# Optimization experiments

Measured on AMD Instinct MI355X. Metric: run time of the kernel, lower is better.

Reference implementation:

```python
import jax, jax.numpy as jnp
import numpy as np

D_MODEL = 128
N_HEADS = 8
D_HEAD = D_MODEL // N_HEADS
D_EDGE = 32
D_GATE = max(D_EDGE * 2, 64)
N_NODES = 50000
N_EDGES = 800000


def setup_inputs() -> dict:
    key = jax.random.key(0)
    ks = jax.random.split(key, 11)
    s = 1.0 / np.sqrt(D_MODEL)
    se = 1.0 / np.sqrt(D_EDGE)
    sg = 1.0 / np.sqrt(D_GATE)
    return {
        "x": jax.random.normal(ks[0], (N_NODES, D_MODEL), jnp.float32),
        "edge_index": jax.random.randint(ks[1], (2, N_EDGES), 0, N_NODES, jnp.int64) if jax.config.jax_enable_x64 else jax.random.randint(ks[1], (2, N_EDGES), 0, N_NODES, jnp.int32),
        "edge_attr": jax.random.normal(ks[2], (N_EDGES, D_EDGE), jnp.float32),
        "W_q": jax.random.normal(ks[3], (D_MODEL, D_MODEL), jnp.float32) * s,
        "W_k": jax.random.normal(ks[4], (D_MODEL, D_MODEL), jnp.float32) * s,
        "W_v": jax.random.normal(ks[5], (D_MODEL, D_MODEL), jnp.float32) * s,
        "W_o": jax.random.normal(ks[6], (D_MODEL, D_MODEL), jnp.float32) * s,
        "W_ek": jax.random.normal(ks[7], (D_EDGE, D_MODEL), jnp.float32) * se,
        "W_ev": jax.random.normal(ks[8], (D_EDGE, D_MODEL), jnp.float32) * se,
        "W_g1": jax.random.normal(ks[9], (D_EDGE, D_GATE), jnp.float32) * se,
        "W_g2": jax.random.normal(ks[10], (D_GATE, N_HEADS), jnp.float32) * sg,
    }


def reference(x, edge_index, edge_attr, W_q, W_k, W_v, W_o, W_ek, W_ev, W_g1, W_g2):
    N = x.shape[0]
    E = edge_attr.shape[0]
    H, D = N_HEADS, D_HEAD
    src, dst = edge_index[0], edge_index[1]

    q = (x @ W_q).reshape(N, H, D)
    k = (x @ W_k).reshape(N, H, D)
    v = (x @ W_v).reshape(N, H, D)

    # per-edge gather + edge-feature enrichment of K, V
    q_e = q[dst]                                        # [E,H,D]
    k_e = k[src] + (edge_attr @ W_ek).reshape(E, H, D)  # [E,H,D]
    v_e = v[src] + (edge_attr @ W_ev).reshape(E, H, D)  # [E,H,D]

    scale = jnp.asarray(np.sqrt(D), x.dtype)
    gate = jax.nn.silu(edge_attr @ W_g1) @ W_g2         # [E,H]
    scores = jnp.sum(q_e * k_e, axis=-1) / scale + gate  # [E,H]

    # 3-pass scatter segment softmax over destination nodes
    m = jax.ops.segment_max(scores, dst, num_segments=N)   # [N,H]
    exp_s = jnp.exp(scores - m[dst])                        # [E,H]
    denom = jax.ops.segment_sum(exp_s, dst, num_segments=N)  # [N,H]
    att = exp_s / (denom[dst] + 1e-9)                       # [E,H]

    out = jax.ops.segment_sum(att[..., None] * v_e, dst, num_segments=N)  # [N,H,D]
    return out.reshape(N, H * D) @ W_o
```

## Files before the change

### kernel.cpp

```cpp
#include <hip/hip_runtime.h>

#define NN 50000
#define NP 50048
#define NE 800000
#define DM 128
#define NH 8
#define DE 32
#define DG 64
#define MAXDEG 64
#define LOG2E 1.44269504088896f
#define SHIFT 16.0f

typedef __attribute__((ext_vector_type(8))) short bf16x8;
typedef __attribute__((ext_vector_type(4))) float f32x4;
typedef __attribute__((ext_vector_type(2))) float f32x2;

__device__ __forceinline__ unsigned short f2bf(float f) {
    unsigned u = __float_as_uint(f);
    unsigned r = u + 0x7FFFu + ((u >> 16) & 1u);
    return (unsigned short)(r >> 16);
}

__global__ void k_prep(const float* __restrict__ Wq, const float* __restrict__ Wk,
                       const float* __restrict__ Wv, unsigned short* __restrict__ wt,
                       const float* __restrict__ Wo, unsigned short* __restrict__ wto,
                       const float* __restrict__ Wek, float* __restrict__ WekT,
                       const float* __restrict__ Wg1, unsigned short* __restrict__ wg1t,
                       const float* __restrict__ Wg2, unsigned short* __restrict__ wg2t,
                       int* __restrict__ cnt) {
    int idx = blockIdx.x * 256 + threadIdx.x;
    if (idx < 3 * DM * DM) {
        int m = idx >> 14, rem = idx & 16383, c = rem >> 7, kk = rem & 127;
        const float* W = m == 0 ? Wq : (m == 1 ? Wk : Wv);
        wt[idx] = f2bf(W[kk * DM + c]);
    }
    if (idx < DM * DM) {
        int c = idx >> 7, kk = idx & 127;
        wto[idx] = f2bf(Wo[kk * DM + c]);
    }
    if (idx < DE * DM) {
        int d = idx >> 5, i = idx & 31;
        WekT[idx] = Wek[i * DM + d];
    }
    if (idx < DG * DE) {
        int c = idx >> 5, kk = idx & 31;
        wg1t[idx] = f2bf(Wg1[kk * DG + c]);
    }
    if (idx < 16 * DG) {
        int c = idx >> 6, kk = idx & 63;
        wg2t[idx] = (c < NH) ? f2bf(Wg2[kk * NH + c]) : (unsigned short)0;
    }
    if (idx < NN) cnt[idx] = 0;
}

__global__ __launch_bounds__(256) void k_qkv(
    const float* __restrict__ x, const unsigned short* __restrict__ wt,
    float* __restrict__ q, unsigned* __restrict__ kvp) {
    int lane = threadIdx.x & 63;
    int w = threadIdx.x >> 6;
    int rt = blockIdx.x * 64 + w * 16;
    int cl = lane & 15;
    int kc = (lane >> 4) * 8;
    bool valid = (rt + cl) < NN;
    bf16x8 a[4];
    #pragma unroll
    for (int ks = 0; ks < 4; ++ks) {
        float4 f0 = make_float4(0.f, 0.f, 0.f, 0.f), f1 = f0;
        if (valid) {
            const float* xp = x + (size_t)(rt + cl) * DM + ks * 32 + kc;
            f0 = *(const float4*)xp;
            f1 = *(const float4*)(xp + 4);
        }
        bf16x8 av;
        av[0] = (short)f2bf(f0.x); av[1] = (short)f2bf(f0.y);
        av[2] = (short)f2bf(f0.z); av[3] = (short)f2bf(f0.w);
        av[4] = (short)f2bf(f1.x); av[5] = (short)f2bf(f1.y);
        av[6] = (short)f2bf(f1.z); av[7] = (short)f2bf(f1.w);
        a[ks] = av;
    }
    int r0w = rt + (lane >> 4) * 4;
    const float QSC = 0.25f * LOG2E;
    #pragma unroll
    for (int m = 0; m < 3; ++m) {
        const unsigned short* wtm = wt + m * DM * DM;
        f32x4 acc[8];
        #pragma unroll
        for (int j = 0; j < 8; ++j) acc[j] = (f32x4){0.f, 0.f, 0.f, 0.f};
        #pragma unroll
        for (int j = 0; j < 8; ++j) {
            #pragma unroll
            for (int ks = 0; ks < 4; ++ks) {
                bf16x8 b = *(const bf16x8*)(wtm + (size_t)(j * 16 + cl) * DM + ks * 32 + kc);
                acc[j] = __builtin_amdgcn_mfma_f32_16x16x32_bf16(a[ks], b, acc[j], 0, 0, 0);
            }
        }
        if (m == 0) {
            #pragma unroll
            for (int j = 0; j < 8; ++j)
                #pragma unroll
                for (int r = 0; r < 4; ++r)
                    q[(size_t)(r0w + r) * DM + j * 16 + cl] = acc[j][r] * QSC;
        } else {
            #pragma unroll
            for (int j = 0; j < 4; ++j)
                #pragma unroll
                for (int r = 0; r < 4; ++r) {
                    unsigned pk = (unsigned)f2bf(acc[j][r]) | ((unsigned)f2bf(acc[j + 4][r]) << 16);
                    kvp[(size_t)(r0w + r) * DM + 2 * (j * 16 + cl) + (m - 1)] = pk;
                }
        }
    }
}

__global__ __launch_bounds__(256) void k_qwek(
    const float* __restrict__ q, const float* __restrict__ WekT,
    unsigned* __restrict__ qwekh) {
    int t = threadIdx.x & 127;
    int sub = threadIdx.x >> 7;
    int h = t >> 4, i2 = t & 15;
    float wk0[16], wk1[16];
    #pragma unroll
    for (int d = 0; d < 16; ++d) {
        wk0[d] = WekT[(h * 16 + d) * 32 + 2 * i2];
        wk1[d] = WekT[(h * 16 + d) * 32 + 2 * i2 + 1];
    }
    for (int n = blockIdx.x * 2 + sub; n < NN; n += gridDim.x * 2) {
        const float4* qr = (const float4*)(q + (size_t)n * DM + h * 16);
        float a0 = 0.f, a1 = 0.f;
        #pragma unroll
        for (int c = 0; c < 4; ++c) {
            float4 qq = qr[c];
            a0 += qq.x * wk0[4*c] + qq.y * wk0[4*c+1] + qq.z * wk0[4*c+2] + qq.w * wk0[4*c+3];
            a1 += qq.x * wk1[4*c] + qq.y * wk1[4*c+1] + qq.z * wk1[4*c+2] + qq.w * wk1[4*c+3];
        }
        qwekh[(size_t)n * 128 + h * 16 + i2] = (unsigned)f2bf(a0) | ((unsigned)f2bf(a1) << 16);
    }
}

__global__ __launch_bounds__(256) void k_edge(
    const float* __restrict__ ea,
    const unsigned short* __restrict__ wg1t, const unsigned short* __restrict__ wg2t,
    const int* __restrict__ ei, int* __restrict__ cnt,
    int2* __restrict__ eb, float2* __restrict__ g2, unsigned* __restrict__ eah) {
    __shared__ unsigned short hls[4][16 * 64];
    int lane = threadIdx.x & 63;
    int wv = threadIdx.x >> 6;
    int e0 = (blockIdx.x * 4 + wv) * 16;
    int cl = lane & 15;
    int g = lane >> 4;
    int kc = g * 8;

    const float* ear = ea + (size_t)(e0 + cl) * DE + kc;
    float4 f0 = *(const float4*)ear;
    float4 f1 = *(const float4*)(ear + 4);
    bf16x8 a;
    a[0] = (short)f2bf(f0.x); a[1] = (short)f2bf(f0.y);
    a[2] = (short)f2bf(f0.z); a[3] = (short)f2bf(f0.w);
    a[4] = (short)f2bf(f1.x); a[5] = (short)f2bf(f1.y);
    a[6] = (short)f2bf(f1.z); a[7] = (short)f2bf(f1.w);
    *(bf16x8*)(eah + (size_t)(e0 + cl) * 16 + kc / 2) = a;

    f32x4 hC[4];
    #pragma unroll
    for (int j = 0; j < 4; ++j) {
        bf16x8 b = *(const bf16x8*)(wg1t + (size_t)(j * 16 + cl) * DE + kc);
        hC[j] = __builtin_amdgcn_mfma_f32_16x16x32_bf16(a, b, (f32x4){0.f, 0.f, 0.f, 0.f}, 0, 0, 0);
    }

    unsigned short* hw = hls[wv];
    #pragma unroll
    for (int j = 0; j < 4; ++j) {
        #pragma unroll
        for (int r = 0; r < 4; ++r) {
            float h = hC[j][r];
            float s = h * __frcp_rn(1.f + __builtin_amdgcn_exp2f(-LOG2E * h));
            int rowE = g * 4 + r;
            int byte = ((rowE * 128) + (j * 16 + cl) * 2) ^ ((rowE & 7) << 4);
            *(unsigned short*)((char*)hw + byte) = f2bf(s);
        }
    }
    __syncthreads();

    int rb0 = ((cl * 128) + g * 16) ^ ((cl & 7) << 4);
    int rb1 = ((cl * 128) + 64 + g * 16) ^ ((cl & 7) << 4);
    bf16x8 a2lo = *(bf16x8*)((char*)hw + rb0);
    bf16x8 a2hi = *(bf16x8*)((char*)hw + rb1);
    bf16x8 b2lo = *(const bf16x8*)(wg2t + (size_t)cl * DG + kc);
    bf16x8 b2hi = *(const bf16x8*)(wg2t + (size_t)cl * DG + 32 + kc);
    f32x4 c2 = __builtin_amdgcn_mfma_f32_16x16x32_bf16(a2lo, b2lo, (f32x4){0.f, 0.f, 0.f, 0.f}, 0, 0, 0);
    c2 = __builtin_amdgcn_mfma_f32_16x16x32_bf16(a2hi, b2hi, c2, 0, 0, 0);

    #pragma unroll
    for (int r = 0; r < 4; ++r) {
        float val = c2[r] * LOG2E - SHIFT;
        float other = __shfl_xor(val, 4);
        if (cl < 4)
            g2[(size_t)(e0 + g * 4 + r) * 4 + cl] = make_float2(val, other);
    }

    if (lane < 16) {
        int e = e0 + lane;
        int src = ei[e], dst = ei[NE + e];
        int slot = atomicAdd(&cnt[dst], 1);
        if (slot < MAXDEG) eb[(size_t)dst * MAXDEG + slot] = make_int2(e, src);
    }
}

#define ECOMP(KV, EAU, GAB, QAB, QWX, QWY, LAB, AAB, EX, EY) {                    \
    unsigned kw = (unsigned)(KV), vw = (unsigned)((KV) >> 32);                    \
    f32x2 kAB = {__uint_as_float(kw << 16), __uint_as_float(kw & 0xFFFF0000u)};   \
    f32x2 vAB = {__uint_as_float(vw << 16), __uint_as_float(vw & 0xFFFF0000u)};   \
    float eax = __uint_as_float((EAU) << 16);                                     \
    float eay = __uint_as_float((EAU) & 0xFFFF0000u);                             \
    f32x2 p = QAB * kAB;                                                          \
    p += (f32x2){eax, eax} * QWX;                                                 \
    p += (f32x2){eay, eay} * QWY;                                                 \
    int t0, t1;                                                                   \
    t0 = __builtin_amdgcn_update_dpp(0, __float_as_int(p.x), 0xB1, 0xF, 0xF, true); \
    t1 = __builtin_amdgcn_update_dpp(0, __float_as_int(p.y), 0xB1, 0xF, 0xF, true); \
    p += (f32x2){__int_as_float(t0), __int_as_float(t1)};                         \
    t0 = __builtin_amdgcn_update_dpp(0, __float_as_int(p.x), 0x4E, 0xF, 0xF, true); \
    t1 = __builtin_amdgcn_update_dpp(0, __float_as_int(p.y), 0x4E, 0xF, 0xF, true); \
    p += (f32x2){__int_as_float(t0), __int_as_float(t1)};                         \
    t0 = __builtin_amdgcn_update_dpp(0, __float_as_int(p.x), 0x141, 0xF, 0xF, true); \
    t1 = __builtin_amdgcn_update_dpp(0, __float_as_int(p.y), 0x141, 0xF, 0xF, true); \
    p += (f32x2){__int_as_float(t0), __int_as_float(t1)};                         \
    t0 = __builtin_amdgcn_update_dpp(0, __float_as_int(p.x), 0x140, 0xF, 0xF, true); \
    t1 = __builtin_amdgcn_update_dpp(0, __float_as_int(p.y), 0x140, 0xF, 0xF, true); \
    p += (f32x2){__int_as_float(t0), __int_as_float(t1)};                         \
    p += GAB;                                                                     \
    f32x2 px = {__builtin_amdgcn_exp2f(p.x), __builtin_amdgcn_exp2f(p.y)};        \
    LAB += px;                                                                    \
    AAB += px * vAB;                                                              \
    EX += (f32x2){px.x, px.x} * (f32x2){eax, eay};                                \
    EY += (f32x2){px.y, px.y} * (f32x2){eax, eay};                                \
}

#define LOADGEN(JIDX, EVV, SVV, KDST, EDST, GDST) {                               \
    int e_ = __builtin_amdgcn_readlane(EVV, JIDX);                                \
    int s_ = __builtin_amdgcn_readlane(SVV, JIDX);                                \
    KDST = kvp[(size_t)s_ * 64 + lane];                                           \
    EDST = eah[(size_t)e_ * 16 + i2];                                             \
    float2 gtmp_ = *(const float2*)(g2f + (size_t)e_ * 8 + hA * 2);               \
    GDST = (f32x2){gtmp_.x, gtmp_.y};                                             \
}

__global__ __launch_bounds__(256) void k_fused(
    const float* __restrict__ q, const unsigned long long* __restrict__ kvp,
    const unsigned* __restrict__ qwekh, const float* __restrict__ g2f,
    const unsigned* __restrict__ eah, const int2* __restrict__ eb,
    const int* __restrict__ cnt, const float* __restrict__ Wev,
    float* __restrict__ outb) {
    int lane = threadIdx.x & 63;
    int gwid = blockIdx.x * 4 + (threadIdx.x >> 6);
    int n0 = gwid * 2, n1 = n0 + 1;
    int hA = lane >> 4;
    int i2 = lane & 15;

    int deg0 = cnt[n0]; deg0 = deg0 > MAXDEG ? MAXDEG : deg0;
    int deg1 = cnt[n1]; deg1 = deg1 > MAXDEG ? MAXDEG : deg1;
    int s0 = lane < deg0 ? lane : 0;
    int s1 = lane < deg1 ? lane : 0;
    int2 t0 = eb[(size_t)n0 * MAXDEG + s0];
    int2 t1 = eb[(size_t)n1 * MAXDEG + s1];
    if (deg0 == 0) { t0.x = 0; t0.y = 0; }
    if (deg1 == 0) { t1.x = 0; t1.y = 0; }
    int ev0 = t0.x, sv0 = t0.y, ev1 = t1.x, sv1 = t1.y;

    f32x2 QAB0 = {q[(size_t)n0 * DM + lane], q[(size_t)n0 * DM + 64 + lane]};
    f32x2 QAB1 = {q[(size_t)n1 * DM + lane], q[(size_t)n1 * DM + 64 + lane]};
    unsigned uA0 = qwekh[(size_t)n0 * 128 + hA * 16 + i2];
    unsigned uB0 = qwekh[(size_t)n0 * 128 + (hA + 4) * 16 + i2];
    unsigned uA1 = qwekh[(size_t)n1 * 128 + hA * 16 + i2];
    unsigned uB1 = qwekh[(size_t)n1 * 128 + (hA + 4) * 16 + i2];
    f32x2 QWX0 = {__uint_as_float(uA0 << 16), __uint_as_float(uB0 << 16)};
    f32x2 QWY0 = {__uint_as_float(uA0 & 0xFFFF0000u), __uint_as_float(uB0 & 0xFFFF0000u)};
    f32x2 QWX1 = {__uint_as_float(uA1 << 16), __uint_as_float(uB1 << 16)};
    f32x2 QWY1 = {__uint_as_float(uA1 & 0xFFFF0000u), __uint_as_float(uB1 & 0xFFFF0000u)};

    f32x2 LAB0 = {0.f, 0.f}, AAB0 = {0.f, 0.f}, EX0 = {0.f, 0.f}, EY0 = {0.f, 0.f};
    f32x2 LAB1 = {0.f, 0.f}, AAB1 = {0.f, 0.f}, EX1 = {0.f, 0.f}, EY1 = {0.f, 0.f};

    int degm = deg0 > deg1 ? deg0 : deg1;

    unsigned long long kvA0, kvA1, kvB0, kvB1;
    unsigned eaA0, eaA1, eaB0, eaB1;
    f32x2 gA0, gA1, gB0, gB1;
    LOADGEN(0, ev0, sv0, kvA0, eaA0, gA0)
    LOADGEN(0, ev1, sv1, kvA1, eaA1, gA1)
    LOADGEN(1, ev0, sv0, kvB0, eaB0, gB0)
    LOADGEN(1, ev1, sv1, kvB1, eaB1, gB1)

    int jmax = degm - 1;
    for (int j = 0; j < degm; j += 2) {
        if (j < deg0) ECOMP(kvA0, eaA0, gA0, QAB0, QWX0, QWY0, LAB0, AAB0, EX0, EY0)
        int jp = j + 2 < jmax ? j + 2 : jmax;
        LOADGEN(jp, ev0, sv0, kvA0, eaA0, gA0)
        if (j < deg1) ECOMP(kvA1, eaA1, gA1, QAB1, QWX1, QWY1, LAB1, AAB1, EX1, EY1)
        LOADGEN(jp, ev1, sv1, kvA1, eaA1, gA1)
        if (j + 1 < deg0) ECOMP(kvB0, eaB0, gB0, QAB0, QWX0, QWY0, LAB0, AAB0, EX0, EY0)
        int jq = j + 3 < jmax ? j + 3 : jmax;
        LOADGEN(jq, ev0, sv0, kvB0, eaB0, gB0)
        if (j + 1 < deg1) ECOMP(kvB1, eaB1, gB1, QAB1, QWX1, QWY1, LAB1, AAB1, EX1, EY1)
        LOADGEN(jq, ev1, sv1, kvB1, eaB1, gB1)
    }

    float e00 = EX0.x, e01 = EX0.y, e02 = EY0.x, e03 = EY0.y;
    float e10 = EX1.x, e11 = EX1.y, e12 = EY1.x, e13 = EY1.y;
    int basel = lane & 48;
    float enA0 = 0.f, enB0 = 0.f, enA1 = 0.f, enB1 = 0.f;
    #pragma unroll
    for (int i = 0; i < DE; i += 2) {
        int sl = basel | (i >> 1);
        float w0A = Wev[i * DM + lane],      w1A = Wev[(i + 1) * DM + lane];
        float w0B = Wev[i * DM + 64 + lane], w1B = Wev[(i + 1) * DM + 64 + lane];
        enA0 += __shfl(e00, sl) * w0A + __shfl(e01, sl) * w1A;
        enB0 += __shfl(e02, sl) * w0B + __shfl(e03, sl) * w1B;
        enA1 += __shfl(e10, sl) * w0A + __shfl(e11, sl) * w1A;
        enB1 += __shfl(e12, sl) * w0B + __shfl(e13, sl) * w1B;
    }
    outb[(size_t)n0 * DM + lane]      = (AAB0.x + enA0) / fmaxf(LAB0.x, 1e-30f);
    outb[(size_t)n0 * DM + 64 + lane] = (AAB0.y + enB0) / fmaxf(LAB0.y, 1e-30f);
    outb[(size_t)n1 * DM + lane]      = (AAB1.x + enA1) / fmaxf(LAB1.x, 1e-30f);
    outb[(size_t)n1 * DM + 64 + lane] = (AAB1.y + enB1) / fmaxf(LAB1.y, 1e-30f);
}

__global__ __launch_bounds__(256) void k_final(
    float* __restrict__ dout, const unsigned short* __restrict__ wto) {
    int lane = threadIdx.x & 63;
    int w = threadIdx.x >> 6;
    int rt = blockIdx.x * 64 + w * 16;
    if (rt >= NN) return;
    int cl = lane & 15;
    int kc = (lane >> 4) * 8;
    bf16x8 a[4];
    #pragma unroll
    for (int ks = 0; ks < 4; ++ks) {
        float4 f0 = *(const float4*)(dout + (size_t)(rt + cl) * DM + ks * 32 + kc);
        float4 f1 = *(const float4*)(dout + (size_t)(rt + cl) * DM + ks * 32 + kc + 4);
        bf16x8 av;
        av[0] = (short)f2bf(f0.x); av[1] = (short)f2bf(f0.y);
        av[2] = (short)f2bf(f0.z); av[3] = (short)f2bf(f0.w);
        av[4] = (short)f2bf(f1.x); av[5] = (short)f2bf(f1.y);
        av[6] = (short)f2bf(f1.z); av[7] = (short)f2bf(f1.w);
        a[ks] = av;
    }
    f32x4 acc[8];
    #pragma unroll
    for (int j = 0; j < 8; ++j) acc[j] = (f32x4){0.f, 0.f, 0.f, 0.f};
    #pragma unroll
    for (int j = 0; j < 8; ++j) {
        #pragma unroll
        for (int ks = 0; ks < 4; ++ks) {
            bf16x8 b = *(const bf16x8*)(wto + (size_t)(j * 16 + cl) * DM + ks * 32 + kc);
            acc[j] = __builtin_amdgcn_mfma_f32_16x16x32_bf16(a[ks], b, acc[j], 0, 0, 0);
        }
    }
    int r0w = rt + (lane >> 4) * 4;
    #pragma unroll
    for (int j = 0; j < 8; ++j)
        #pragma unroll
        for (int r = 0; r < 4; ++r)
            dout[(size_t)(r0w + r) * DM + j * 16 + cl] = acc[j][r];
}

extern "C" void kernel_launch(void* const* d_in, const int* in_sizes, int n_in,
                              void* d_out, int out_size, void* d_ws, size_t ws_size,
                              hipStream_t stream) {
    const float* x   = (const float*)d_in[0];
    const int*   ei  = (const int*)d_in[1];
    const float* ea  = (const float*)d_in[2];
    const float* Wq  = (const float*)d_in[3];
    const float* Wk  = (const float*)d_in[4];
    const float* Wv  = (const float*)d_in[5];
    const float* Wo  = (const float*)d_in[6];
    const float* Wek = (const float*)d_in[7];
    const float* Wev = (const float*)d_in[8];
    const float* Wg1 = (const float*)d_in[9];
    const float* Wg2 = (const float*)d_in[10];
    float* dout = (float*)d_out;

    float* ws = (float*)d_ws;
    float* q        = ws;
    unsigned* kvp   = (unsigned*)(q + (size_t)NP * DM);
    unsigned* qwekh = kvp + (size_t)NP * DM;
    float* g2f      = (float*)(qwekh + (size_t)NN * 128);
    int2* eb        = (int2*)(g2f + (size_t)NE * 8);
    unsigned* eah   = (unsigned*)(eb + (size_t)NN * MAXDEG);
    int* cnt        = (int*)(eah + (size_t)NE * 16);
    unsigned short* wt = (unsigned short*)(cnt + NN);
    unsigned short* wto = wt + 3 * DM * DM;
    unsigned short* wg1t = wto + DM * DM;
    unsigned short* wg2t = wg1t + DG * DE;
    float* WekT     = (float*)(wg2t + 16 * DG);

    k_prep<<<(NN + 255) / 256, 256, 0, stream>>>(Wq, Wk, Wv, wt, Wo, wto, Wek, WekT,
                                                 Wg1, wg1t, Wg2, wg2t, cnt);
    k_qkv<<<NP / 64, 256, 0, stream>>>(x, wt, q, kvp);
    k_qwek<<<512, 256, 0, stream>>>(q, WekT, qwekh);
    k_edge<<<NE / 64, 256, 0, stream>>>(ea, wg1t, wg2t, ei, cnt, eb, (float2*)g2f, eah);
    k_fused<<<NN / 8, 256, 0, stream>>>(q, (const unsigned long long*)kvp,
                                        qwekh, g2f, eah, eb, cnt, Wev, dout);
    k_final<<<(NN + 63) / 64, 256, 0, stream>>>(dout, wto);
}
```

Before: 282.2 us.

## Sort nodes by in-degree before fused attention to balance wave work

Adds a counting sort of destination nodes by clamped in-degree (histogram, serial scan, atomic placement) and makes the fused kernel process nodes in that order. The goal is to pair nodes of similar degree within waves and blocks, cutting idle lanes and tail imbalance in the per-edge loop. It adds three small kernel launches, including a single-thread scan, and scatters node accesses so q, qwekh and output rows lose contiguity.

```diff
diff --git a/kernel.cpp b/kernel.cpp
--- a/kernel.cpp
+++ b/kernel.cpp
@@ -8,6 +8,7 @@
 #define DE 32
 #define DG 64
 #define MAXDEG 64
+#define NBINS 65
 #define LOG2E 1.44269504088896f
 #define SHIFT 16.0f
 
@@ -27,7 +28,7 @@
                        const float* __restrict__ Wek, float* __restrict__ WekT,
                        const float* __restrict__ Wg1, unsigned short* __restrict__ wg1t,
                        const float* __restrict__ Wg2, unsigned short* __restrict__ wg2t,
-                       int* __restrict__ cnt) {
+                       int* __restrict__ cnt, int* __restrict__ bhist) {
     int idx = blockIdx.x * 256 + threadIdx.x;
     if (idx < 3 * DM * DM) {
         int m = idx >> 14, rem = idx & 16383, c = rem >> 7, kk = rem & 127;
@@ -51,6 +52,7 @@
         wg2t[idx] = (c < NH) ? f2bf(Wg2[kk * NH + c]) : (unsigned short)0;
     }
     if (idx < NN) cnt[idx] = 0;
+    if (idx < NBINS) bhist[idx] = 0;
 }
 
 __global__ __launch_bounds__(256) void k_qkv(
@@ -203,6 +205,31 @@
         int src = ei[e], dst = ei[NE + e];
         int slot = atomicAdd(&cnt[dst], 1);
         if (slot < MAXDEG) eb[(size_t)dst * MAXDEG + slot] = make_int2(e, src);
+    }
+}
+
+__global__ void k_hist(const int* __restrict__ cnt, int* __restrict__ bhist) {
+    int idx = blockIdx.x * 256 + threadIdx.x;
+    if (idx < NN) {
+        int d = cnt[idx]; d = d > MAXDEG ? MAXDEG : d;
+        atomicAdd(&bhist[d], 1);
+    }
+}
+
+__global__ void k_hscan(const int* __restrict__ bhist, int* __restrict__ bcur) {
+    if (threadIdx.x == 0 && blockIdx.x == 0) {
+        int run = 0;
+        for (int i = 0; i < NBINS; ++i) { bcur[i] = run; run += bhist[i]; }
+    }
+}
+
+__global__ void k_place(const int* __restrict__ cnt, int* __restrict__ bcur,
+                        int* __restrict__ sorted) {
+    int idx = blockIdx.x * 256 + threadIdx.x;
+    if (idx < NN) {
+        int d = cnt[idx]; d = d > MAXDEG ? MAXDEG : d;
+        int pos = atomicAdd(&bcur[d], 1);
+        sorted[pos] = idx;
     }
 }
 
@@ -249,11 +276,11 @@
     const float* __restrict__ q, const unsigned long long* __restrict__ kvp,
     const unsigned* __restrict__ qwekh, const float* __restrict__ g2f,
     const unsigned* __restrict__ eah, const int2* __restrict__ eb,
-    const int* __restrict__ cnt, const float* __restrict__ Wev,
-    float* __restrict__ outb) {
+    const int* __restrict__ cnt, const int* __restrict__ sorted,
+    const float* __restrict__ Wev, float* __restrict__ outb) {
     int lane = threadIdx.x & 63;
     int gwid = blockIdx.x * 4 + (threadIdx.x >> 6);
-    int n0 = gwid * 2, n1 = n0 + 1;
+    int n0 = sorted[gwid * 2], n1 = sorted[gwid * 2 + 1];
     int hA = lane >> 4;
     int i2 = lane & 15;
 
@@ -388,18 +415,24 @@
     int2* eb        = (int2*)(g2f + (size_t)NE * 8);
     unsigned* eah   = (unsigned*)(eb + (size_t)NN * MAXDEG);
     int* cnt        = (int*)(eah + (size_t)NE * 16);
-    unsigned short* wt = (unsigned short*)(cnt + NN);
+    int* sorted     = cnt + NN;
+    int* bhist      = sorted + NN;
+    int* bcur       = bhist + NBINS;
+    unsigned short* wt = (unsigned short*)(bcur + NBINS);
     unsigned short* wto = wt + 3 * DM * DM;
     unsigned short* wg1t = wto + DM * DM;
     unsigned short* wg2t = wg1t + DG * DE;
     float* WekT     = (float*)(wg2t + 16 * DG);
 
     k_prep<<<(NN + 255) / 256, 256, 0, stream>>>(Wq, Wk, Wv, wt, Wo, wto, Wek, WekT,
-                                                 Wg1, wg1t, Wg2, wg2t, cnt);
+                                                 Wg1, wg1t, Wg2, wg2t, cnt, bhist);
     k_qkv<<<NP / 64, 256, 0, stream>>>(x, wt, q, kvp);
     k_qwek<<<512, 256, 0, stream>>>(q, WekT, qwekh);
     k_edge<<<NE / 64, 256, 0, stream>>>(ea, wg1t, wg2t, ei, cnt, eb, (float2*)g2f, eah);
+    k_hist<<<(NN + 255) / 256, 256, 0, stream>>>(cnt, bhist);
+    k_hscan<<<1, 64, 0, stream>>>(bhist, bcur);
+    k_place<<<(NN + 255) / 256, 256, 0, stream>>>(cnt, bcur, sorted);
     k_fused<<<NN / 8, 256, 0, stream>>>(q, (const unsigned long long*)kvp,
-                                        qwekh, g2f, eah, eb, cnt, Wev, dout);
+                                        qwekh, g2f, eah, eb, cnt, sorted, Wev, dout);
     k_final<<<(NN + 63) / 64, 256, 0, stream>>>(dout, wto);
 }
```

Measured after the change: 553.7 us. 1.96x slower.
